# Optimization experiments

Measured on AMD Instinct MI355X. Metric: run time of the kernel, lower is better.

## Reference

```python
import jax, jax.numpy as jnp
import numpy as np

DIM = 256
NUM_HEAD = 8
HEAD_DIM = DIM // NUM_HEAD
SCALE = HEAD_DIM ** -0.5


def setup_inputs() -> dict:
    key = jax.random.key(0)
    ks = jax.random.split(key, 8)
    B, NQ, NK = 8, 512, 4096
    state = jax.random.normal(ks[0], (B, NQ, DIM), dtype=jnp.float32)
    pointcloud = jax.random.normal(ks[1], (B, NK, DIM), dtype=jnp.float32)
    s = 0.02
    Wq = jax.random.normal(ks[2], (DIM, DIM), dtype=jnp.float32) * s
    bq = jnp.zeros((DIM,), dtype=jnp.float32)
    Wkv = jax.random.normal(ks[3], (DIM, 2 * DIM), dtype=jnp.float32) * s
    bkv = jnp.zeros((2 * DIM,), dtype=jnp.float32)
    Wo = jax.random.normal(ks[4], (DIM, DIM), dtype=jnp.float32) * s
    bo = jnp.zeros((DIM,), dtype=jnp.float32)
    return {"state": state, "pointcloud": pointcloud, "Wq": Wq, "bq": bq,
            "Wkv": Wkv, "bkv": bkv, "Wo": Wo, "bo": bo}


def reference(state, pointcloud, Wq, bq, Wkv, bkv, Wo, bo):
    # q: [b, nq, dim]; kv: [b, nk, 2*dim]
    q = state @ Wq + bq
    kv = pointcloud @ Wkv + bkv
    k, v = jnp.split(kv, 2, axis=-1)

    def split_heads(x):
        b, n, _ = x.shape
        return x.reshape(b, n, NUM_HEAD, HEAD_DIM).transpose(0, 2, 1, 3)  # b h n d

    q, k, v = split_heads(q), split_heads(k), split_heads(v)
    attn = jnp.einsum('bhqd,bhkd->bhqk', q, k) * SCALE
    attn = jax.nn.softmax(attn, axis=-1)
    out = jnp.einsum('bhqk,bhkd->bhqd', attn, v)
    b, h, nq, d = out.shape
    out = out.transpose(0, 2, 1, 3).reshape(b, nq, h * d)
    return out @ Wo + bo
```

## Files before the change

### kernel.cpp

```cpp
#include <hip/hip_runtime.h>

typedef unsigned short u16;
typedef unsigned int   u32;
typedef __bf16 bf16x8 __attribute__((ext_vector_type(8)));
typedef float  f32x4  __attribute__((ext_vector_type(4)));
typedef float  f32x16 __attribute__((ext_vector_type(16)));
typedef u32    u32x4  __attribute__((ext_vector_type(4)));
typedef u16    u16x8  __attribute__((ext_vector_type(8)));

#define DEVINL __device__ __forceinline__

DEVINL void glds16(const void* g, void* l) {
  __builtin_amdgcn_global_load_lds((const __attribute__((address_space(1))) u32*)g,
                                   (__attribute__((address_space(3))) u32*)l, 16, 0, 0);
}

DEVINL u16 f2bf(float f) {
  u32 u = __builtin_bit_cast(u32, f);
  u32 r = u + 0x7fffu + ((u >> 16) & 1u);
  return (u16)(r >> 16);
}

__global__ __launch_bounds__(256) void castw_k(const float* __restrict__ Wq,
                                               const float* __restrict__ Wkv,
                                               const float* __restrict__ Wo,
                                               u16* __restrict__ WqT, u16* __restrict__ WkvT,
                                               u16* __restrict__ WoT) {
  int i = blockIdx.x * 256 + threadIdx.x;
  if (i < 65536) {
    int n = i >> 8, k = i & 255;
    WqT[i] = f2bf(Wq[k * 256 + n]);
  } else if (i < 196608) {
    int j = i - 65536; int n = j >> 8, k = j & 255;
    WkvT[j] = f2bf(Wkv[k * 512 + n]);
  } else {
    int j = i - 196608; int n = j >> 8, k = j & 255;
    WoT[j] = f2bf(Wo[k * 256 + n]);
  }
}

template<int EPI, int ASRC, bool XCDSWZ>
DEVINL void gemm_body(const void* __restrict__ Ap, const u16* __restrict__ Bt,
                      const float* __restrict__ bias, void* __restrict__ Cp,
                      void* __restrict__ C2p, const float* __restrict__ Dp,
                      u16* As, u16* Bs, int N, int nmt, float scale, int bid, int nblk) {
  const int K = 256;
  int tid = threadIdx.x, lane = tid & 63, w = tid >> 6;
  int g = lane >> 4, ln15 = lane & 15;
  int mt, nt;
  if (XCDSWZ) {
    int u = (bid & 7) * (nblk >> 3) + (bid >> 3);
    mt = u >> 2; nt = u & 3;
  } else {
    mt = bid % nmt; nt = bid / nmt;
  }
  int arow0 = mt * 128, bcol0 = nt * 128;
  int wr = w >> 1, wc = w & 1;
  f32x4 acc[4][4] = {};

  for (int kt = 0; kt < 4; ++kt) {
    if (kt) __syncthreads();
    if (ASRC == 1) {
      const float* A = (const float*)Ap;
      #pragma unroll
      for (int i = 0; i < 4; ++i) {
        int c = i * 256 + tid; int row = c >> 3, k8 = c & 7;
        const float* src = A + (size_t)(arow0 + row) * K + kt * 64 + k8 * 8;
        f32x4 f0 = *(const f32x4*)src, f1 = *(const f32x4*)(src + 4);
        u16x8 hh;
        hh[0]=f2bf(f0[0]); hh[1]=f2bf(f0[1]); hh[2]=f2bf(f0[2]); hh[3]=f2bf(f0[3]);
        hh[4]=f2bf(f1[0]); hh[5]=f2bf(f1[1]); hh[6]=f2bf(f1[2]); hh[7]=f2bf(f1[3]);
        int idx = row * 8 + (k8 ^ (row & 7));
        *(u16x8*)&As[idx * 8] = hh;
      }
    } else if (ASRC == 2) {
      const float* A = (const float*)Ap;
      #pragma unroll
      for (int i = 0; i < 4; ++i) {
        int c = i * 256 + tid; int row = c >> 3, k8 = c & 7;
        int col0 = kt * 64 + k8 * 8;
        int h = col0 >> 5;
        size_t base = (size_t)(arow0 + row) * 256 + col0;
        f32x4 lo = {}, hi4 = {};
        float dsum = 0.f;
        #pragma unroll
        for (int ss = 0; ss < 4; ++ss) {
          const float* p = A + ss * 1048576;
          lo  += *(const f32x4*)(p + base);
          hi4 += *(const f32x4*)(p + base + 4);
          dsum += Dp[(ss * 4096 + arow0 + row) * 8 + h];
        }
        float inv = 1.0f / dsum;
        u16x8 hh;
        hh[0]=f2bf(lo[0]*inv);  hh[1]=f2bf(lo[1]*inv);  hh[2]=f2bf(lo[2]*inv);  hh[3]=f2bf(lo[3]*inv);
        hh[4]=f2bf(hi4[0]*inv); hh[5]=f2bf(hi4[1]*inv); hh[6]=f2bf(hi4[2]*inv); hh[7]=f2bf(hi4[3]*inv);
        int idx = row * 8 + (k8 ^ (row & 7));
        *(u16x8*)&As[idx * 8] = hh;
      }
    } else {
      const u16* A = (const u16*)Ap;
      #pragma unroll
      for (int i = 0; i < 4; ++i) {
        int c = i * 256 + tid; int row = c >> 3, seg = c & 7;
        const u16* src = A + (size_t)(arow0 + row) * K + kt * 64 + (seg ^ (row & 7)) * 8;
        glds16(src, (char*)As + (i * 256 + w * 64) * 16);
      }
    }
    #pragma unroll
    for (int i = 0; i < 4; ++i) {
      int c = i * 256 + tid; int row = c >> 3, seg = c & 7;
      const u16* src = Bt + (size_t)(bcol0 + row) * K + kt * 64 + (seg ^ (row & 7)) * 8;
      glds16(src, (char*)Bs + (i * 256 + w * 64) * 16);
    }
    __syncthreads();
    #pragma unroll
    for (int kk = 0; kk < 2; ++kk) {
      bf16x8 af[4], bfr[4];
      #pragma unroll
      for (int mi = 0; mi < 4; ++mi) {
        int row = wr * 64 + mi * 16 + ln15;
        int idx = row * 8 + ((kk * 4 + g) ^ (row & 7));
        af[mi] = __builtin_bit_cast(bf16x8, *(const u32x4*)&As[idx * 8]);
      }
      #pragma unroll
      for (int ni = 0; ni < 4; ++ni) {
        int row = wc * 64 + ni * 16 + ln15;
        int idx = row * 8 + ((kk * 4 + g) ^ (row & 7));
        bfr[ni] = __builtin_bit_cast(bf16x8, *(const u32x4*)&Bs[idx * 8]);
      }
      #pragma unroll
      for (int mi = 0; mi < 4; ++mi)
        #pragma unroll
        for (int ni = 0; ni < 4; ++ni)
          acc[mi][ni] = __builtin_amdgcn_mfma_f32_16x16x32_bf16(af[mi], bfr[ni], acc[mi][ni], 0, 0, 0);
    }
  }
  #pragma unroll
  for (int mi = 0; mi < 4; ++mi) {
    #pragma unroll
    for (int ni = 0; ni < 4; ++ni) {
      int col = bcol0 + wc * 64 + ni * 16 + ln15;
      float bv = bias[col];
      #pragma unroll
      for (int r = 0; r < 4; ++r) {
        int row = arow0 + wr * 64 + mi * 16 + g * 4 + r;
        float v = acc[mi][ni][r] + bv;
        if (EPI == 0) {
          ((float*)Cp)[(size_t)row * N + col] = v;
        } else if (EPI == 1) {
          ((u16*)Cp)[(size_t)row * N + col] = f2bf(v * scale);
        } else {
          int b = row >> 12, nk = row & 4095;
          if (col < 256) {
            int h = col >> 5, d = col & 31;
            ((u16*)Cp)[((size_t)((b << 3) + h) * 4096 + nk) * 32 + d] = f2bf(v);
          } else {
            int c2 = col - 256; int h = c2 >> 5, d = c2 & 31;
            ((u16*)C2p)[((size_t)((b << 3) + h) * 4096 + nk) * 32 + d] = f2bf(v);
          }
        }
      }
    }
  }
}

__global__ __launch_bounds__(256) void gemm12_k(const float* __restrict__ state,
                                                const float* __restrict__ pc,
                                                const u16* __restrict__ WqT,
                                                const u16* __restrict__ WkvT,
                                                const float* __restrict__ bq,
                                                const float* __restrict__ bkv,
                                                u16* __restrict__ qbuf, u16* __restrict__ kbuf,
                                                u16* __restrict__ vbuf, float qscl) {
  __shared__ __align__(16) u16 As[128 * 64];
  __shared__ __align__(16) u16 Bs[128 * 64];
  int bid = blockIdx.x;
  if (bid < 1024) {
    gemm_body<2, 1, true >(pc, WkvT, bkv, kbuf, vbuf, nullptr, As, Bs, 512, 256, 1.f, bid, 1024);
  } else {
    gemm_body<1, 1, false>(state, WqT, bq, qbuf, nullptr, nullptr, As, Bs, 256, 32, qscl, bid - 1024, 64);
  }
}

__global__ __launch_bounds__(256) void gemm3_k(const float* __restrict__ Op,
                                               const u16* __restrict__ WoT,
                                               const float* __restrict__ bo,
                                               float* __restrict__ out,
                                               const float* __restrict__ Dp) {
  __shared__ __align__(16) u16 As[128 * 64];
  __shared__ __align__(16) u16 Bs[128 * 64];
  gemm_body<0, 2, false>(Op, WoT, bo, out, nullptr, Dp, As, Bs, 256, 32, 1.f, blockIdx.x, 64);
}

__global__ __launch_bounds__(256) void attn_k(const u16* __restrict__ qb,
                                              const u16* __restrict__ kb,
                                              const u16* __restrict__ vb,
                                              float* __restrict__ Op,
                                              float* __restrict__ Dp) {
  __shared__ __align__(16) u16 Ks[2][2048];
  __shared__ __align__(16) u16 Vt[2][2048];
  int tid = threadIdx.x, lane = tid & 63, w = tid >> 6;
  int hi = lane >> 5, ln31 = lane & 31;
  int bid = blockIdx.x;
  int qblk = bid >> 8, r2 = bid & 255, bh = r2 >> 2, s = r2 & 3;
  int b = bh >> 3, h = bh & 7;
  const u16* khead = kb + ((size_t)bh * 4096 + s * 1024) * 32;
  const u16* vhead = vb + ((size_t)bh * 4096 + s * 1024) * 32;
  int qrow0 = b * 512 + qblk * 128 + w * 32;

  bf16x8 qf[2];
  #pragma unroll
  for (int ks = 0; ks < 2; ++ks) {
    const u16* src = qb + (size_t)(qrow0 + ln31) * 256 + h * 32 + ks * 16 + hi * 8;
    qf[ks] = __builtin_bit_cast(bf16x8, *(const u32x4*)src);
  }

  f32x16 O = {};
  float den = 0.f;
  int vrow = tid >> 2, vdc = tid & 3;

  auto loadV = [&](int t) -> u32x4 {
    return *(const u32x4*)(vhead + ((size_t)t * 64 + vrow) * 32 + vdc * 8);
  };
  auto stage = [&](int buf, int t, u32x4 vv) {
    glds16(khead + ((size_t)t * 64 + lane) * 32 + w * 8, (char*)&Ks[buf][0] + w * 1024);
    u16x8 us = __builtin_bit_cast(u16x8, vv);
    #pragma unroll
    for (int j = 0; j < 8; ++j) {
      int d = vdc * 8 + j;
      int cs = (vrow >> 3) ^ j ^ (vdc << 1);
      Vt[buf][d * 64 + cs * 8 + (vrow & 7)] = us[j];
    }
  };

  u32x4 vv = loadV(0);
  stage(0, 0, vv);
  vv = loadV(1);
  __syncthreads();

  for (int t = 0; t < 16; ++t) {
    int buf = t & 1;
    if (t + 1 < 16) {
      stage(buf ^ 1, t + 1, vv);
      vv = loadV(t + 2 < 16 ? t + 2 : 15);
    }
    f32x16 sT[2] = {};
    #pragma unroll
    for (int ks = 0; ks < 2; ++ks) {
      #pragma unroll
      for (int mt = 0; mt < 2; ++mt) {
        const u16* ka = &Ks[buf][((ks * 2 + hi) * 64 + mt * 32 + ln31) * 8];
        bf16x8 kf = __builtin_bit_cast(bf16x8, *(const u32x4*)ka);
        sT[mt] = __builtin_amdgcn_mfma_f32_32x32x16_bf16(kf, qf[ks], sT[mt], 0, 0, 0);
      }
    }
    u32 pa[4][4];
    #pragma unroll
    for (int mt = 0; mt < 2; ++mt) {
      float p[16];
      #pragma unroll
      for (int r = 0; r < 16; ++r) p[r] = __builtin_amdgcn_exp2f(sT[mt][r]);
      #pragma unroll
      for (int r = 0; r < 16; ++r) den += p[r];
      u32 pk0[4], pk1[4];
      #pragma unroll
      for (int c = 0; c < 4; ++c) {
        asm("v_cvt_pk_bf16_f32 %0, %1, %2" : "=v"(pk0[c]) : "v"(p[4*c+0]), "v"(p[4*c+1]));
        asm("v_cvt_pk_bf16_f32 %0, %1, %2" : "=v"(pk1[c]) : "v"(p[4*c+2]), "v"(p[4*c+3]));
      }
      u32 a0 = pk0[0], b0 = pk0[1];
      asm("v_permlane32_swap_b32 %0, %1" : "+v"(a0), "+v"(b0));
      u32 a1 = pk1[0], b1 = pk1[1];
      asm("v_permlane32_swap_b32 %0, %1" : "+v"(a1), "+v"(b1));
      u32 a2 = pk0[2], b2 = pk0[3];
      asm("v_permlane32_swap_b32 %0, %1" : "+v"(a2), "+v"(b2));
      u32 a3 = pk1[2], b3 = pk1[3];
      asm("v_permlane32_swap_b32 %0, %1" : "+v"(a3), "+v"(b3));
      pa[mt*2+0][0] = a0; pa[mt*2+0][1] = a1; pa[mt*2+0][2] = b0; pa[mt*2+0][3] = b1;
      pa[mt*2+1][0] = a2; pa[mt*2+1][1] = a3; pa[mt*2+1][2] = b2; pa[mt*2+1][3] = b3;
    }
    #pragma unroll
    for (int kst = 0; kst < 4; ++kst) {
      int cs = (kst * 2 + hi) ^ (ln31 & 7) ^ ((ln31 >> 3) << 1);
      const u16* va = &Vt[buf][ln31 * 64 + cs * 8];
      bf16x8 vf = __builtin_bit_cast(bf16x8, *(const u32x4*)va);
      u32x4 paw = {pa[kst][0], pa[kst][1], pa[kst][2], pa[kst][3]};
      O = __builtin_amdgcn_mfma_f32_32x32x16_bf16(__builtin_bit_cast(bf16x8, paw), vf, O, 0, 0, 0);
    }
    __syncthreads();
  }

  den += __shfl_xor(den, 32);
  float* op = Op + (size_t)s * 1048576;
  #pragma unroll
  for (int r = 0; r < 16; ++r) {
    int qr = 8 * (r >> 2) + 4 * hi + (r & 3);
    op[(size_t)(qrow0 + qr) * 256 + h * 32 + ln31] = O[r];
  }
  if (lane < 32) Dp[(size_t)(s * 4096 + qrow0 + ln31) * 8 + h] = den;
}

extern "C" void kernel_launch(void* const* d_in, const int* in_sizes, int n_in,
                              void* d_out, int out_size, void* d_ws, size_t ws_size,
                              hipStream_t stream) {
  const float* state = (const float*)d_in[0];
  const float* pc    = (const float*)d_in[1];
  const float* Wq    = (const float*)d_in[2];
  const float* bq    = (const float*)d_in[3];
  const float* Wkv   = (const float*)d_in[4];
  const float* bkv   = (const float*)d_in[5];
  const float* Wo    = (const float*)d_in[6];
  const float* bo    = (const float*)d_in[7];
  char* ws = (char*)d_ws;
  u16*   WqT  = (u16*)(ws);
  u16*   WkvT = (u16*)(ws + 131072);
  u16*   WoT  = (u16*)(ws + 393216);
  u16*   qb   = (u16*)(ws + 524288);
  u16*   kb   = (u16*)(ws + 2621440);
  u16*   vb   = (u16*)(ws + 19398656);
  float* Op   = (float*)(ws + 36175872);
  float* Dp   = (float*)(ws + 52953088);

  castw_k<<<1024, 256, 0, stream>>>(Wq, Wkv, Wo, WqT, WkvT, WoT);
  const float QSCL = 0.17677669529663687f * 1.4426950408889634f;
  gemm12_k<<<1088, 256, 0, stream>>>(state, pc, WqT, WkvT, bq, bkv, qb, kb, vb, QSCL);
  attn_k<<<1024, 256, 0, stream>>>(qb, kb, vb, Op, Dp);
  gemm3_k<<<64, 256, 0, stream>>>(Op, WoT, bo, (float*)d_out, Dp);
}
```

Before: 171.3 us.

## Pre-cast GEMM inputs to bf16 and double-buffer the GEMM K loop

Moves the fp32-to-bf16 conversion of state and pointcloud into a separate prep kernel, so all GEMMs load bf16 tiles asynchronously through global_load_lds. The GEMM K loop becomes double-buffered, issuing the next tile's loads before computing the current one. The split-K reduction and normalisation of the attention output moves out of the output GEMM into its own reduce kernel. This costs an extra kernel launch plus an extra write and read of the bf16 copies of the inputs, and doubles LDS per GEMM block, which may lower occupancy.

```diff
diff --git a/kernel.cpp b/kernel.cpp
--- a/kernel.cpp
+++ b/kernel.cpp
@@ -21,29 +21,56 @@
   return (u16)(r >> 16);
 }
 
-__global__ __launch_bounds__(256) void castw_k(const float* __restrict__ Wq,
-                                               const float* __restrict__ Wkv,
-                                               const float* __restrict__ Wo,
-                                               u16* __restrict__ WqT, u16* __restrict__ WkvT,
-                                               u16* __restrict__ WoT) {
-  int i = blockIdx.x * 256 + threadIdx.x;
-  if (i < 65536) {
-    int n = i >> 8, k = i & 255;
-    WqT[i] = f2bf(Wq[k * 256 + n]);
-  } else if (i < 196608) {
-    int j = i - 65536; int n = j >> 8, k = j & 255;
-    WkvT[j] = f2bf(Wkv[k * 512 + n]);
+DEVINL u32 cvtpk(float lo, float hi) {
+  u32 r;
+  asm("v_cvt_pk_bf16_f32 %0, %1, %2" : "=v"(r) : "v"(lo), "v"(hi));
+  return r;
+}
+
+DEVINL u16x8 cvt8(f32x4 a, f32x4 b) {
+  u32x4 r = {cvtpk(a[0], a[1]), cvtpk(a[2], a[3]), cvtpk(b[0], b[1]), cvtpk(b[2], b[3])};
+  return __builtin_bit_cast(u16x8, r);
+}
+
+__global__ __launch_bounds__(256) void prep_k(const float* __restrict__ Wq,
+                                              const float* __restrict__ Wkv,
+                                              const float* __restrict__ Wo,
+                                              const float* __restrict__ state,
+                                              const float* __restrict__ pc,
+                                              u16* __restrict__ WqT, u16* __restrict__ WkvT,
+                                              u16* __restrict__ WoT, u16* __restrict__ sb,
+                                              u16* __restrict__ pb) {
+  int bid = blockIdx.x, tid = threadIdx.x;
+  if (bid < 1024) {
+    int i = bid * 256 + tid;
+    if (i < 65536) {
+      int n = i >> 8, k = i & 255;
+      WqT[i] = f2bf(Wq[k * 256 + n]);
+    } else if (i < 196608) {
+      int j = i - 65536; int n = j >> 8, k = j & 255;
+      WkvT[j] = f2bf(Wkv[k * 512 + n]);
+    } else {
+      int j = i - 196608; int n = j >> 8, k = j & 255;
+      WoT[j] = f2bf(Wo[k * 256 + n]);
+    }
+  } else if (bid < 1536) {
+    size_t u = (size_t)(bid - 1024) * 256 + tid;
+    f32x4 a = *(const f32x4*)(state + u * 8);
+    f32x4 b = *(const f32x4*)(state + u * 8 + 4);
+    *(u16x8*)(sb + u * 8) = cvt8(a, b);
   } else {
-    int j = i - 196608; int n = j >> 8, k = j & 255;
-    WoT[j] = f2bf(Wo[k * 256 + n]);
-  }
-}
-
-template<int EPI, int ASRC, bool XCDSWZ>
-DEVINL void gemm_body(const void* __restrict__ Ap, const u16* __restrict__ Bt,
+    size_t u = (size_t)(bid - 1536) * 256 + tid;
+    f32x4 a = *(const f32x4*)(pc + u * 8);
+    f32x4 b = *(const f32x4*)(pc + u * 8 + 4);
+    *(u16x8*)(pb + u * 8) = cvt8(a, b);
+  }
+}
+
+template<int EPI, bool XCDSWZ>
+DEVINL void gemm_body(const u16* __restrict__ A, const u16* __restrict__ Bt,
                       const float* __restrict__ bias, void* __restrict__ Cp,
-                      void* __restrict__ C2p, const float* __restrict__ Dp,
-                      u16* As, u16* Bs, int N, int nmt, float scale, int bid, int nblk) {
+                      void* __restrict__ C2p, u16* As, u16* Bs,
+                      int N, int nmt, float scale, int bid, int nblk) {
   const int K = 256;
   int tid = threadIdx.x, lane = tid & 63, w = tid >> 6;
   int g = lane >> 4, ln15 = lane & 15;
@@ -58,61 +85,24 @@
   int wr = w >> 1, wc = w & 1;
   f32x4 acc[4][4] = {};
 
-  for (int kt = 0; kt < 4; ++kt) {
-    if (kt) __syncthreads();
-    if (ASRC == 1) {
-      const float* A = (const float*)Ap;
-      #pragma unroll
-      for (int i = 0; i < 4; ++i) {
-        int c = i * 256 + tid; int row = c >> 3, k8 = c & 7;
-        const float* src = A + (size_t)(arow0 + row) * K + kt * 64 + k8 * 8;
-        f32x4 f0 = *(const f32x4*)src, f1 = *(const f32x4*)(src + 4);
-        u16x8 hh;
-        hh[0]=f2bf(f0[0]); hh[1]=f2bf(f0[1]); hh[2]=f2bf(f0[2]); hh[3]=f2bf(f0[3]);
-        hh[4]=f2bf(f1[0]); hh[5]=f2bf(f1[1]); hh[6]=f2bf(f1[2]); hh[7]=f2bf(f1[3]);
-        int idx = row * 8 + (k8 ^ (row & 7));
-        *(u16x8*)&As[idx * 8] = hh;
-      }
-    } else if (ASRC == 2) {
-      const float* A = (const float*)Ap;
-      #pragma unroll
-      for (int i = 0; i < 4; ++i) {
-        int c = i * 256 + tid; int row = c >> 3, k8 = c & 7;
-        int col0 = kt * 64 + k8 * 8;
-        int h = col0 >> 5;
-        size_t base = (size_t)(arow0 + row) * 256 + col0;
-        f32x4 lo = {}, hi4 = {};
-        float dsum = 0.f;
-        #pragma unroll
-        for (int ss = 0; ss < 4; ++ss) {
-          const float* p = A + ss * 1048576;
-          lo  += *(const f32x4*)(p + base);
-          hi4 += *(const f32x4*)(p + base + 4);
-          dsum += Dp[(ss * 4096 + arow0 + row) * 8 + h];
-        }
-        float inv = 1.0f / dsum;
-        u16x8 hh;
-        hh[0]=f2bf(lo[0]*inv);  hh[1]=f2bf(lo[1]*inv);  hh[2]=f2bf(lo[2]*inv);  hh[3]=f2bf(lo[3]*inv);
-        hh[4]=f2bf(hi4[0]*inv); hh[5]=f2bf(hi4[1]*inv); hh[6]=f2bf(hi4[2]*inv); hh[7]=f2bf(hi4[3]*inv);
-        int idx = row * 8 + (k8 ^ (row & 7));
-        *(u16x8*)&As[idx * 8] = hh;
-      }
-    } else {
-      const u16* A = (const u16*)Ap;
-      #pragma unroll
-      for (int i = 0; i < 4; ++i) {
-        int c = i * 256 + tid; int row = c >> 3, seg = c & 7;
-        const u16* src = A + (size_t)(arow0 + row) * K + kt * 64 + (seg ^ (row & 7)) * 8;
-        glds16(src, (char*)As + (i * 256 + w * 64) * 16);
-      }
-    }
+  auto stage = [&](int buf, int kt) {
     #pragma unroll
     for (int i = 0; i < 4; ++i) {
       int c = i * 256 + tid; int row = c >> 3, seg = c & 7;
-      const u16* src = Bt + (size_t)(bcol0 + row) * K + kt * 64 + (seg ^ (row & 7)) * 8;
-      glds16(src, (char*)Bs + (i * 256 + w * 64) * 16);
-    }
-    __syncthreads();
+      glds16(A + (size_t)(arow0 + row) * K + kt * 64 + (seg ^ (row & 7)) * 8,
+             (char*)As + (size_t)buf * 16384 + (i * 256 + w * 64) * 16);
+      glds16(Bt + (size_t)(bcol0 + row) * K + kt * 64 + (seg ^ (row & 7)) * 8,
+             (char*)Bs + (size_t)buf * 16384 + (i * 256 + w * 64) * 16);
+    }
+  };
+
+  stage(0, 0);
+  __syncthreads();
+  for (int kt = 0; kt < 4; ++kt) {
+    int buf = kt & 1;
+    if (kt < 3) stage(buf ^ 1, kt + 1);
+    const u16* Ab = As + buf * 8192;
+    const u16* Bb = Bs + buf * 8192;
     #pragma unroll
     for (int kk = 0; kk < 2; ++kk) {
       bf16x8 af[4], bfr[4];
@@ -120,13 +110,13 @@
       for (int mi = 0; mi < 4; ++mi) {
         int row = wr * 64 + mi * 16 + ln15;
         int idx = row * 8 + ((kk * 4 + g) ^ (row & 7));
-        af[mi] = __builtin_bit_cast(bf16x8, *(const u32x4*)&As[idx * 8]);
+        af[mi] = __builtin_bit_cast(bf16x8, *(const u32x4*)&Ab[idx * 8]);
       }
       #pragma unroll
       for (int ni = 0; ni < 4; ++ni) {
         int row = wc * 64 + ni * 16 + ln15;
         int idx = row * 8 + ((kk * 4 + g) ^ (row & 7));
-        bfr[ni] = __builtin_bit_cast(bf16x8, *(const u32x4*)&Bs[idx * 8]);
+        bfr[ni] = __builtin_bit_cast(bf16x8, *(const u32x4*)&Bb[idx * 8]);
       }
       #pragma unroll
       for (int mi = 0; mi < 4; ++mi)
@@ -134,6 +124,7 @@
         for (int ni = 0; ni < 4; ++ni)
           acc[mi][ni] = __builtin_amdgcn_mfma_f32_16x16x32_bf16(af[mi], bfr[ni], acc[mi][ni], 0, 0, 0);
     }
+    __syncthreads();
   }
   #pragma unroll
   for (int mi = 0; mi < 4; ++mi) {
@@ -164,32 +155,52 @@
   }
 }
 
-__global__ __launch_bounds__(256) void gemm12_k(const float* __restrict__ state,
-                                                const float* __restrict__ pc,
+__global__ __launch_bounds__(256) void gemm12_k(const u16* __restrict__ sb,
+                                                const u16* __restrict__ pb,
                                                 const u16* __restrict__ WqT,
                                                 const u16* __restrict__ WkvT,
                                                 const float* __restrict__ bq,
                                                 const float* __restrict__ bkv,
                                                 u16* __restrict__ qbuf, u16* __restrict__ kbuf,
                                                 u16* __restrict__ vbuf, float qscl) {
-  __shared__ __align__(16) u16 As[128 * 64];
-  __shared__ __align__(16) u16 Bs[128 * 64];
+  __shared__ __align__(16) u16 As[2 * 8192];
+  __shared__ __align__(16) u16 Bs[2 * 8192];
   int bid = blockIdx.x;
   if (bid < 1024) {
-    gemm_body<2, 1, true >(pc, WkvT, bkv, kbuf, vbuf, nullptr, As, Bs, 512, 256, 1.f, bid, 1024);
+    gemm_body<2, true >(pb, WkvT, bkv, kbuf, vbuf, As, Bs, 512, 256, 1.f, bid, 1024);
   } else {
-    gemm_body<1, 1, false>(state, WqT, bq, qbuf, nullptr, nullptr, As, Bs, 256, 32, qscl, bid - 1024, 64);
-  }
-}
-
-__global__ __launch_bounds__(256) void gemm3_k(const float* __restrict__ Op,
+    gemm_body<1, false>(sb, WqT, bq, qbuf, nullptr, As, Bs, 256, 32, qscl, bid - 1024, 64);
+  }
+}
+
+__global__ __launch_bounds__(256) void gemm3_k(const u16* __restrict__ ob,
                                                const u16* __restrict__ WoT,
                                                const float* __restrict__ bo,
-                                               float* __restrict__ out,
-                                               const float* __restrict__ Dp) {
-  __shared__ __align__(16) u16 As[128 * 64];
-  __shared__ __align__(16) u16 Bs[128 * 64];
-  gemm_body<0, 2, false>(Op, WoT, bo, out, nullptr, Dp, As, Bs, 256, 32, 1.f, blockIdx.x, 64);
+                                               float* __restrict__ out) {
+  __shared__ __align__(16) u16 As[2 * 8192];
+  __shared__ __align__(16) u16 Bs[2 * 8192];
+  gemm_body<0, false>(ob, WoT, bo, out, nullptr, As, Bs, 256, 32, 1.f, blockIdx.x, 64);
+}
+
+__global__ __launch_bounds__(256) void reduce_k(const float* __restrict__ Op,
+                                                const float* __restrict__ Dp,
+                                                u16* __restrict__ ob) {
+  size_t u = (size_t)blockIdx.x * 256 + threadIdx.x;
+  int row = (int)(u >> 5), q8 = (int)(u & 31);
+  int h = q8 >> 2;
+  size_t base = u * 8;
+  f32x4 lo = {}, hi = {};
+  float dsum = 0.f;
+  #pragma unroll
+  for (int ss = 0; ss < 4; ++ss) {
+    const float* p = Op + (size_t)ss * 1048576;
+    lo += *(const f32x4*)(p + base);
+    hi += *(const f32x4*)(p + base + 4);
+    dsum += Dp[((size_t)ss * 4096 + row) * 8 + h];
+  }
+  float inv = 1.0f / dsum;
+  lo *= inv; hi *= inv;
+  *(u16x8*)(ob + base) = cvt8(lo, hi);
 }
 
 __global__ __launch_bounds__(256) void attn_k(const u16* __restrict__ qb,
@@ -265,8 +276,8 @@
       u32 pk0[4], pk1[4];
       #pragma unroll
       for (int c = 0; c < 4; ++c) {
-        asm("v_cvt_pk_bf16_f32 %0, %1, %2" : "=v"(pk0[c]) : "v"(p[4*c+0]), "v"(p[4*c+1]));
-        asm("v_cvt_pk_bf16_f32 %0, %1, %2" : "=v"(pk1[c]) : "v"(p[4*c+2]), "v"(p[4*c+3]));
+        pk0[c] = cvtpk(p[4*c+0], p[4*c+1]);
+        pk1[c] = cvtpk(p[4*c+2], p[4*c+3]);
       }
       u32 a0 = pk0[0], b0 = pk0[1];
       asm("v_permlane32_swap_b32 %0, %1" : "+v"(a0), "+v"(b0));
@@ -315,15 +326,19 @@
   u16*   WqT  = (u16*)(ws);
   u16*   WkvT = (u16*)(ws + 131072);
   u16*   WoT  = (u16*)(ws + 393216);
-  u16*   qb   = (u16*)(ws + 524288);
-  u16*   kb   = (u16*)(ws + 2621440);
-  u16*   vb   = (u16*)(ws + 19398656);
-  float* Op   = (float*)(ws + 36175872);
-  float* Dp   = (float*)(ws + 52953088);
-
-  castw_k<<<1024, 256, 0, stream>>>(Wq, Wkv, Wo, WqT, WkvT, WoT);
+  u16*   sb   = (u16*)(ws + 524288);
+  u16*   pb   = (u16*)(ws + 2621440);
+  u16*   qb   = (u16*)(ws + 19398656);
+  u16*   kb   = (u16*)(ws + 21495808);
+  u16*   vb   = (u16*)(ws + 38273024);
+  u16*   ob   = (u16*)(ws + 55050240);
+  float* Op   = (float*)(ws + 57147392);
+  float* Dp   = (float*)(ws + 73924608);
+
+  prep_k<<<5632, 256, 0, stream>>>(Wq, Wkv, Wo, state, pc, WqT, WkvT, WoT, sb, pb);
   const float QSCL = 0.17677669529663687f * 1.4426950408889634f;
-  gemm12_k<<<1088, 256, 0, stream>>>(state, pc, WqT, WkvT, bq, bkv, qb, kb, vb, QSCL);
+  gemm12_k<<<1088, 256, 0, stream>>>(sb, pb, WqT, WkvT, bq, bkv, qb, kb, vb, QSCL);
   attn_k<<<1024, 256, 0, stream>>>(qb, kb, vb, Op, Dp);
-  gemm3_k<<<64, 256, 0, stream>>>(Op, WoT, bo, (float*)d_out, Dp);
-}
+  reduce_k<<<512, 256, 0, stream>>>(Op, Dp, ob);
+  gemm3_k<<<64, 256, 0, stream>>>(ob, WoT, bo, (float*)d_out);
+}
```

Measured after the change: 156.8 us. -8.5%, faster.
